# Optimization experiments

Hardware: AMD Instinct MI355X
Metric: run time of the kernel (lower is better)

## Reference

```python
import jax, jax.numpy as jnp
import numpy as np

N, C, T, V, O, S, R = 32, 64, 256, 25, 192, 3, 8  # batch, in_ch, time, joints, out_ch, subsets, rel_ch


def setup_inputs() -> dict:
    key = jax.random.key(0)
    ks = jax.random.split(key, 20)
    w = lambda i, shape: (jax.random.normal(ks[i], shape, jnp.float32) * 0.05)
    return {
        "x": jax.random.normal(ks[0], (N, C, T, V), jnp.float32),
        "spd_A": jax.random.normal(ks[1], (V, V), jnp.float32) * 0.1,
        "A3": jax.random.normal(ks[2], (S, V, V), jnp.float32) * 0.1,
        "A6": jax.random.normal(ks[3], (6, V, V), jnp.float32) * 0.1,
        "conv1_w": w(4, (S, R, C)), "conv1_b": jnp.zeros((S, R), jnp.float32),
        "conv2_w": w(5, (S, R, C)), "conv2_b": jnp.zeros((S, R), jnp.float32),
        "conv4_w": w(6, (S, O, R)), "conv4_b": jnp.zeros((S, O), jnp.float32),
        "conv3_w": w(7, (S, O, C)), "conv3_b": jnp.zeros((S, O), jnp.float32),
        "alpha": jnp.full((1,), 0.5, jnp.float32),
        "beta": jnp.full((1,), 0.5, jnp.float32),
        "gamma": jnp.full((1,), 0.5, jnp.float32),
        "bn_w": jnp.ones((O,), jnp.float32), "bn_b": jnp.zeros((O,), jnp.float32),
        "down_w": w(8, (O, C)), "down_b": jnp.zeros((O,), jnp.float32),
        "dbn_w": jnp.ones((O,), jnp.float32), "dbn_b": jnp.zeros((O,), jnp.float32),
    }


def _bn(y, w, b):
    # BatchNorm2d in training mode: stats over (N, T, V) per channel, biased var
    mu = y.mean(axis=(0, 2, 3), keepdims=True)
    var = ((y - mu) ** 2).mean(axis=(0, 2, 3), keepdims=True)
    return (y - mu) * jax.lax.rsqrt(var + 1e-5) * w[None, :, None, None] + b[None, :, None, None]


def reference(x, spd_A, A3, A6, conv1_w, conv1_b, conv2_w, conv2_b, conv4_w, conv4_b,
              conv3_w, conv3_b, alpha, beta, gamma, bn_w, bn_b, down_w, down_b, dbn_w, dbn_b):
    out_c = conv4_w.shape[1]
    # A6 expanded: (out//6, 6, V, V) -> (out, V, V); contiguous-view == tile along channel blocks
    A6_ex = jnp.tile(A6, (out_c // 6, 1, 1))  # (O, V, V)
    # 1x1 conv then temporal mean == conv on temporal mean (linear op commutes)
    xm = x.mean(axis=2)  # (N, C, V)
    x1 = jnp.einsum('ncv,src->nsrv', xm, conv1_w) + conv1_b[None, :, :, None]
    x2 = jnp.einsum('ncv,src->nsrv', xm, conv2_w) + conv2_b[None, :, :, None]
    d = jnp.tanh(x1[..., :, None] - x2[..., None, :])  # (N, S, R, V, V)
    A_dyn = jnp.einsum('nsruv,sor->nsouv', d, conv4_w) + conv4_b[None, :, :, None, None]
    A_at = (A_dyn * alpha + A3[None, :, None, :, :]
            + A6_ex[None, None] * beta + spd_A[None, None, None] * gamma)  # (N, S, O, V, V)
    # CTRGC_2: x3 = conv3(x); einsum 'ncuv,nctv->nctu', summed over subsets
    x3 = jnp.einsum('nctv,soc->nsotv', x, conv3_w) + conv3_b[None, :, :, None, None]
    y = jnp.einsum('nsouv,nsotv->notu', A_at, x3)  # (N, O, T, V)
    y = _bn(y, bn_w, bn_b)
    xd = jnp.einsum('nctv,oc->notv', x, down_w) + down_b[None, :, None, None]
    y = jax.nn.relu(y + _bn(xd, dbn_w, dbn_b))
    return y
```

## Files before the change

kernel.cpp:

```cpp
#include <hip/hip_runtime.h>

#define N_ 32
#define C_ 64
#define T_ 256
#define V_ 25
#define O_ 192
#define S_ 3
#define R_ 8
#define VV (V_*V_)
#define TV (T_*V_)
#define RP 26
#define TRP (T_*RP)

typedef unsigned short u16;
typedef unsigned int u32;
typedef __attribute__((ext_vector_type(4))) u16 u16x4;
typedef __attribute__((ext_vector_type(8))) u16 u16x8;
typedef __attribute__((ext_vector_type(4))) u32 u32x4;
typedef __attribute__((ext_vector_type(8))) __bf16 bf16x8;
typedef __attribute__((ext_vector_type(4))) float f32x4;

#define WS_A2F_U 0
#define WS_XQ_U  (18874368)
#define WS_XD_U  (18874368 + 13631488)
#define WS_YB_U  (18874368 + 13631488 + 39321600)
#define WS_XM_F   (55574528)
#define WS_RS_F   (55574528 + 51200)
#define WS_STAT_F (55574528 + 51200 + 153600)
#define WS_COEF_F (55574528 + 51200 + 153600 + 768)

__device__ __forceinline__ u16 f2b(float f) {
    return __builtin_bit_cast(u16, (__bf16)f);
}
__device__ __forceinline__ float b2f(u16 u) {
    return __builtin_bit_cast(float, ((unsigned)u) << 16);
}
__device__ __forceinline__ f32x4 mfma16(bf16x8 a, bf16x8 b, f32x4 c) {
    return __builtin_amdgcn_mfma_f32_16x16x32_bf16(a, b, c, 0, 0, 0);
}

__global__ void k0_xq(const float* __restrict__ x, u16* __restrict__ xq) {
    __shared__ float tile[64][52];
    int bid = blockIdx.x;
    int n = bid >> 7, tb = bid & 127;
    int t0 = tb * 2;
    int tid = threadIdx.x;
    const float2* xp = (const float2*)(x + (size_t)n * C_ * TV + t0 * 25);
    for (int p = tid; p < 1600; p += 256) {
        int c = p / 25, q = p % 25;
        float2 f2 = xp[(size_t)c * 3200 + q];
        tile[c][q * 2] = f2.x;
        tile[c][q * 2 + 1] = f2.y;
    }
    __syncthreads();
    for (int p = tid; p < 832; p += 256) {
        int row = p >> 4, c4g = p & 15;
        int t = row >= RP, v = row - t * RP;
        u16x4 w;
        #pragma unroll
        for (int i = 0; i < 4; ++i) {
            int co = ((c4g & 3) << 4) + ((c4g >> 2) << 2) + i;
            w[i] = (v < 25) ? f2b(tile[co][t * 25 + v]) : (u16)0;
        }
        *(u16x4*)&xq[((size_t)n * TRP + tb * 52 + row) * 64 + c4g * 4] = w;
    }
}

__global__ void k1_xm(const u16* __restrict__ xq, float* __restrict__ xm_out) {
    __shared__ float ps[256];
    int bid = blockIdx.x;
    int n = bid / 25, v = bid % 25;
    int tid = threadIdx.x;
    int cg = tid & 63, tg = tid >> 6;
    const u16* p = xq + (size_t)n * TRP * 64 + ((size_t)(tg * 64 * RP + v)) * 64 + cg;
    float s = 0.f;
    for (int t = 0; t < 64; ++t) {
        s += b2f(*p);
        p += RP * 64;
    }
    ps[tid] = s;
    __syncthreads();
    if (tid < 64) {
        float tot = ps[tid] + ps[64 + tid] + ps[128 + tid] + ps[192 + tid];
        int c4g = tid >> 2, i = tid & 3;
        int co = ((c4g & 3) << 4) + ((c4g >> 2) << 2) + i;
        xm_out[((size_t)n * C_ + co) * V_ + v] = tot * (1.f / T_);
    }
}

__global__ void k2_a2f(const float* __restrict__ spd, const float* __restrict__ A3,
                       const float* __restrict__ A6,
                       const float* __restrict__ w1, const float* __restrict__ b1,
                       const float* __restrict__ w2, const float* __restrict__ b2,
                       const float* __restrict__ w4, const float* __restrict__ b4,
                       const float* __restrict__ b3,
                       const float* __restrict__ alpha, const float* __restrict__ beta,
                       const float* __restrict__ gamma,
                       u16* __restrict__ a2f, const float* __restrict__ xmbuf,
                       float* __restrict__ rs_tot) {
    __shared__ float xm[C_ * V_];
    __shared__ float x1s[R_ * V_], x2s[R_ * V_];
    __shared__ float dm[R_ * VV];
    __shared__ float a3s[VV], sps[VV];
    __shared__ float aatw[4][2 * VV];
    int bid = blockIdx.x;
    int n = bid / 24;
    int rem = bid % 24;
    int s = rem / 8, og = rem % 8;
    int tid = threadIdx.x, wid = tid >> 6, lane = tid & 63;
    const float* xmg = xmbuf + (size_t)n * C_ * V_;
    for (int p = tid; p < C_ * V_; p += 256) xm[p] = xmg[p];
    for (int p = tid; p < VV; p += 256) { a3s[p] = A3[s * VV + p]; sps[p] = spd[p]; }
    __syncthreads();
    if (tid < R_ * V_) {
        int r = tid / V_, v = tid % V_;
        float acc1 = b1[s * R_ + r], acc2 = b2[s * R_ + r];
        for (int c = 0; c < C_; ++c) {
            float xv = xm[c * V_ + v];
            acc1 += xv * w1[(s * R_ + r) * C_ + c];
            acc2 += xv * w2[(s * R_ + r) * C_ + c];
        }
        x1s[tid] = acc1; x2s[tid] = acc2;
    }
    __syncthreads();
    for (int p = tid; p < R_ * VV; p += 256) {
        int r = p / VV, uv = p % VV, u = uv / V_, v = uv % V_;
        dm[p] = tanhf(x1s[r * V_ + u] - x2s[r * V_ + v]);
    }
    __syncthreads();
    float al = alpha[0], be = beta[0], ga = gamma[0];
    float* aat = aatw[wid];
    for (int opi = 0; opi < 3; ++opi) {
        int op = wid * 3 + opi;
        int o0 = og * 24 + op * 2;
        float w4v[2][R_], b4v[2];
        #pragma unroll
        for (int oo = 0; oo < 2; ++oo) {
            b4v[oo] = b4[s * O_ + o0 + oo];
            #pragma unroll
            for (int r = 0; r < R_; ++r)
                w4v[oo][r] = w4[((size_t)(s * O_ + o0 + oo)) * R_ + r];
        }
        const float* a6p0 = A6 + ((o0 % 6) * VV);
        for (int p = lane; p < 2 * VV; p += 64) {
            int oo = p / VV, pp = p - oo * VV;
            float acc = b4v[oo];
            #pragma unroll
            for (int r = 0; r < R_; ++r) acc += dm[r * VV + pp] * w4v[oo][r];
            aat[p] = al * acc + a3s[pp] + ga * sps[pp] + be * a6p0[oo * VV + pp];
        }
        if (lane < 2 * V_) {
            int oo = lane / V_, u = lane - oo * V_;
            float rs = 0.f;
            for (int v = 0; v < V_; ++v) rs += aat[oo * VV + u * V_ + v];
            atomicAdd(&rs_tot[((size_t)(n * O_ + o0 + oo)) * V_ + u],
                      b3[s * O_ + o0 + oo] * rs);
        }
        #pragma unroll
        for (int it = 0; it < 4; ++it) {
            int idx = it * 64 + lane;
            int oo = idx >> 7, l2 = idx & 127, cu = l2 >> 6, l = l2 & 63;
            int u = cu * 16 + (l & 15);
            u16x8 w;
            #pragma unroll
            for (int j = 0; j < 8; ++j) {
                int v = ((j >> 2) << 4) + ((l >> 4) << 2) + (j & 3);
                float val = 0.f;
                if (u < V_ && v < V_) val = aat[oo * VV + u * V_ + v];
                w[j] = f2b(val);
            }
            size_t idxg = ((((size_t)(n * O_ + o0 + oo)) * S_ + s) * 2 + cu) * 64 + l;
            ((u16x8*)a2f)[idxg] = w;
        }
    }
}

#define OSTR_B 2504
#define SSTR_B 832
#define BUF_B  20064

__global__ __launch_bounds__(256, 3)
void k3_main(const u16* __restrict__ xq,
             const float* __restrict__ w3, const float* __restrict__ dw,
             const float* __restrict__ db,
             const u16* __restrict__ a2f, const float* __restrict__ rs_tot,
             u16* __restrict__ yb16, u16* __restrict__ xdws,
             float* __restrict__ stats) {
    __shared__ char x3Lb[2 * BUF_B];
    __shared__ u16 xdst[8 * 416];
    __shared__ u16 ystage[8 * 400];
    int orig = blockIdx.x;
    int bid = (orig & 7) * 96 + (orig >> 3);
    int n = bid / 24;
    int o0 = (bid % 24) * 8;
    int tid = threadIdx.x, wid = tid >> 6, lane = tid & 63;
    int lr = lane & 15, lg = lane >> 4;
    int colt = wid & 1;
    int rt0 = (wid >> 1) * 13;

    for (int p = tid; p < 2 * BUF_B / 16; p += 256) ((u32x4*)x3Lb)[p] = u32x4{0,0,0,0};

    const float* wsrc = (colt == 0)
        ? w3 + ((size_t)((lr >> 3) * O_ + o0 + (lr & 7))) * C_
        : ((lr < 8) ? w3 + ((size_t)(2 * O_ + o0 + lr)) * C_
                    : dw + ((size_t)(o0 + lr - 8)) * C_);
    bf16x8 bw[2];
    #pragma unroll
    for (int ks = 0; ks < 2; ++ks) {
        u16x8 tmp;
        #pragma unroll
        for (int j = 0; j < 8; ++j) {
            int c = ks * 32 + (lg << 2) + (j & 3) + ((j >> 2) << 4);
            tmp[j] = f2b(wsrc[c]);
        }
        bw[ks] = __builtin_bit_cast(bf16x8, tmp);
    }
    float dbv = (colt == 1 && lr >= 8) ? db[o0 + lr - 8] : 0.f;

    int wo = (colt == 0) ? (lr & 7) : lr;
    int wsb = (colt == 0) ? (lr >> 3) : 2;
    int colbyte = wo * OSTR_B + wsb * SSTR_B;

    const bf16x8* a2v = (const bf16x8*)a2f;
    bf16x8 Bh[2][6];
    float rsb0[2], rsb1[2];
    #pragma unroll
    for (int oi = 0; oi < 2; ++oi) {
        int o = o0 + (wid << 1) + oi;
        const bf16x8* bp = a2v + ((size_t)(n * O_ + o)) * 6 * 64 + lane;
        #pragma unroll
        for (int q = 0; q < 6; ++q) Bh[oi][q] = bp[(size_t)q * 64];
        const float* rsp = rs_tot + ((size_t)(n * O_ + o)) * V_;
        rsb0[oi] = rsp[lr];
        rsb1[oi] = (lr < 9) ? rsp[16 + lr] : 0.f;
    }

    float sy1[2] = {0, 0}, sy2[2] = {0, 0};
    float sd1 = 0.f, sd2 = 0.f;
    const u16* xbn = xq + (size_t)n * TRP * 64;
    int rdw = 13 * lr + 2 * lg;
    char* buf = x3Lb;
    int t0 = 0;

    auto tl = [&](int ch, int j, u16x8& A0, u16x8& A1) {
        const u16* p = xbn + ((size_t)(ch * 16) * RP + (size_t)((rt0 + j) * 16 + lr)) * 64
                       + (lg << 4);
        A0 = *(const u16x8*)p;
        A1 = *(const u16x8*)(p + 8);
    };
    auto proc = [&](int rt, u16x8 A0, u16x8 A1) {
        f32x4 acc = {0.f, 0.f, 0.f, 0.f};
        acc = mfma16(__builtin_bit_cast(bf16x8, A0), bw[0], acc);
        acc = mfma16(__builtin_bit_cast(bf16x8, A1), bw[1], acc);
        int rbase = rt * 16 + (lg << 2);
        if (colt == 0 || lr < 8) {
            u16x4 w;
            #pragma unroll
            for (int reg = 0; reg < 4; ++reg) w[reg] = f2b(acc[reg]);
            *(u16x4*)(buf + colbyte + rbase * 2) = w;
        } else {
            u16x4 w;
            #pragma unroll
            for (int reg = 0; reg < 4; ++reg) {
                int rr = rbase + reg;
                int t = rr / RP, v = rr - t * RP;
                float val = acc[reg] + dbv;
                w[reg] = f2b(val);
                if (v < 25) { sd1 += val; sd2 += val * val; }
            }
            *(u16x4*)&xdst[(lr - 8) * 416 + rbase] = w;
        }
    };

    __syncthreads();

    u16x8 p0a, p0b, p1a, p1b, p2a, p2b, p3a, p3b;
    tl(0, 0, p0a, p0b); tl(0, 1, p1a, p1b); tl(0, 2, p2a, p2b); tl(0, 3, p3a, p3b);

    for (int ch = 0; ch < 16; ++ch) {
        t0 = ch * 16;
        buf = x3Lb + (ch & 1) * BUF_B;
        proc(rt0 + 0, p0a, p0b);
        proc(rt0 + 1, p1a, p1b);
        proc(rt0 + 2, p2a, p2b);
        proc(rt0 + 3, p3a, p3b);
        for (int j = 4; j < 13; ++j) {
            u16x8 A0, A1;
            tl(ch, j, A0, A1);
            proc(rt0 + j, A0, A1);
        }
        if (ch < 15) {
            tl(ch + 1, 0, p0a, p0b); tl(ch + 1, 1, p1a, p1b);
            tl(ch + 1, 2, p2a, p2b); tl(ch + 1, 3, p3a, p3b);
        }
        __syncthreads();
        #pragma unroll
        for (int oi = 0; oi < 2; ++oi) {
            int ol = (wid << 1) + oi;
            const u32* L = (const u32*)(buf + ol * OSTR_B);
            f32x4 acc0 = {0, 0, 0, 0}, acc1 = {0, 0, 0, 0};
            #pragma unroll
            for (int s = 0; s < 3; ++s) {
                const u32* Ls = L + s * 208 + rdw;
                u32 d0 = Ls[0], d1 = Ls[1], d8 = Ls[8], d9 = Ls[9];
                bf16x8 A = __builtin_bit_cast(bf16x8, u32x4{d0, d1, d8, d9});
                acc0 = mfma16(A, Bh[oi][s * 2 + 0], acc0);
                acc1 = mfma16(A, Bh[oi][s * 2 + 1], acc1);
            }
            int ylb = ol * 400 + (lg << 2) * 25;
            #pragma unroll
            for (int reg = 0; reg < 4; ++reg) {
                float v0 = acc0[reg] + rsb0[oi];
                ystage[ylb + reg * 25 + lr] = f2b(v0);
                sy1[oi] += v0; sy2[oi] += v0 * v0;
                if (lr < 9) {
                    float v1 = acc1[reg] + rsb1[oi];
                    ystage[ylb + reg * 25 + 16 + lr] = f2b(v1);
                    sy1[oi] += v1; sy2[oi] += v1 * v1;
                }
            }
        }
        {
            size_t ygb = (size_t)(n * O_ + o0) * TV + (size_t)t0 * V_;
            for (int q = lane; q < 100; q += 64) {
                int sel = q >= 50;
                int ol2 = (wid << 1) + sel;
                int j = q - sel * 50;
                u16x8 pk = *(const u16x8*)&ystage[ol2 * 400 + j * 8];
                *(u16x8*)&yb16[ygb + (size_t)ol2 * TV + j * 8] = pk;
            }
        }
        if (colt == 1) {
            int tofs = (wid >> 1) * 8;
            size_t gdb = (size_t)(n * O_ + o0) * TV + (size_t)(t0 + tofs) * V_;
            for (int q = lane; q < 200; q += 64) {
                int o = q / 25, w = q - o * 25;
                int g0 = w * 8;
                int tl2 = g0 / 25, v = g0 - tl2 * 25;
                u16x8 pk;
                #pragma unroll
                for (int k = 0; k < 8; ++k) {
                    pk[k] = xdst[o * 416 + (tofs + tl2) * RP + v];
                    if (++v == 25) { v = 0; ++tl2; }
                }
                *(u16x8*)&xdws[gdb + (size_t)o * TV + g0] = pk;
            }
        }
    }
    #pragma unroll
    for (int oi = 0; oi < 2; ++oi) {
        float v1 = sy1[oi], v2 = sy2[oi];
        #pragma unroll
        for (int m = 1; m < 64; m <<= 1) {
            v1 += __shfl_xor(v1, m);
            v2 += __shfl_xor(v2, m);
        }
        if (lane == 0) {
            atomicAdd(&stats[0 * O_ + o0 + (wid << 1) + oi], v1);
            atomicAdd(&stats[1 * O_ + o0 + (wid << 1) + oi], v2);
        }
    }
    if (colt == 1) {
        float v1 = sd1, v2 = sd2;
        v1 += __shfl_xor(v1, 16); v2 += __shfl_xor(v2, 16);
        v1 += __shfl_xor(v1, 32); v2 += __shfl_xor(v2, 32);
        if (lane >= 8 && lane < 16) {
            atomicAdd(&stats[2 * O_ + o0 + lane - 8], v1);
            atomicAdd(&stats[3 * O_ + o0 + lane - 8], v2);
        }
    }
}

__global__ void k4_coef(const float* __restrict__ bn_w, const float* __restrict__ bn_b,
                        const float* __restrict__ dbn_w, const float* __restrict__ dbn_b,
                        const float* __restrict__ stats, float* __restrict__ coef) {
    int o = threadIdx.x;
    if (o >= O_) return;
    float inv = 1.f / (float)(N_ * T_ * V_);
    float mu_y = stats[o] * inv;
    float var_y = stats[O_ + o] * inv - mu_y * mu_y;
    float ay = bn_w[o] * rsqrtf(var_y + 1e-5f);
    float by = bn_b[o] - mu_y * ay;
    float mu_d = stats[2 * O_ + o] * inv;
    float var_d = stats[3 * O_ + o] * inv - mu_d * mu_d;
    float ad = dbn_w[o] * rsqrtf(var_d + 1e-5f);
    float bd = dbn_b[o] - mu_d * ad;
    coef[o] = ay; coef[O_ + o] = by; coef[2 * O_ + o] = ad; coef[3 * O_ + o] = bd;
}

__global__ void k5_final(float* __restrict__ out, const u16* __restrict__ yb,
                         const u16* __restrict__ xd, const float* __restrict__ cf) {
    size_t total = (size_t)N_ * O_ * TV / 8;
    for (size_t i = blockIdx.x * (size_t)blockDim.x + threadIdx.x; i < total;
         i += (size_t)gridDim.x * blockDim.x) {
        int o = (int)((i / 800) % O_);
        float ay = cf[o], by = cf[O_ + o], ad = cf[2 * O_ + o], bd = cf[3 * O_ + o];
        u16x8 yv = ((const u16x8*)yb)[i];
        u16x8 dv = ((const u16x8*)xd)[i];
        float4 r0, r1;
        r0.x = fmaxf(ay * b2f(yv[0]) + by + ad * b2f(dv[0]) + bd, 0.f);
        r0.y = fmaxf(ay * b2f(yv[1]) + by + ad * b2f(dv[1]) + bd, 0.f);
        r0.z = fmaxf(ay * b2f(yv[2]) + by + ad * b2f(dv[2]) + bd, 0.f);
        r0.w = fmaxf(ay * b2f(yv[3]) + by + ad * b2f(dv[3]) + bd, 0.f);
        r1.x = fmaxf(ay * b2f(yv[4]) + by + ad * b2f(dv[4]) + bd, 0.f);
        r1.y = fmaxf(ay * b2f(yv[5]) + by + ad * b2f(dv[5]) + bd, 0.f);
        r1.z = fmaxf(ay * b2f(yv[6]) + by + ad * b2f(dv[6]) + bd, 0.f);
        r1.w = fmaxf(ay * b2f(yv[7]) + by + ad * b2f(dv[7]) + bd, 0.f);
        ((float4*)out)[2 * i] = r0;
        ((float4*)out)[2 * i + 1] = r1;
    }
}

extern "C" void kernel_launch(void* const* d_in, const int* in_sizes, int n_in,
                              void* d_out, int out_size, void* d_ws, size_t ws_size,
                              hipStream_t stream) {
    const float* x     = (const float*)d_in[0];
    const float* spd   = (const float*)d_in[1];
    const float* A3    = (const float*)d_in[2];
    const float* A6    = (const float*)d_in[3];
    const float* w1    = (const float*)d_in[4];
    const float* b1    = (const float*)d_in[5];
    const float* w2    = (const float*)d_in[6];
    const float* b2    = (const float*)d_in[7];
    const float* w4    = (const float*)d_in[8];
    const float* b4    = (const float*)d_in[9];
    const float* w3    = (const float*)d_in[10];
    const float* b3    = (const float*)d_in[11];
    const float* alpha = (const float*)d_in[12];
    const float* beta  = (const float*)d_in[13];
    const float* gamma = (const float*)d_in[14];
    const float* bn_w  = (const float*)d_in[15];
    const float* bn_b  = (const float*)d_in[16];
    const float* dw    = (const float*)d_in[17];
    const float* db    = (const float*)d_in[18];
    const float* dbn_w = (const float*)d_in[19];
    const float* dbn_b = (const float*)d_in[20];
    float* out = (float*)d_out;
    u16*   wsu = (u16*)d_ws;
    float* wsf = (float*)d_ws;

    u16* a2f  = wsu + WS_A2F_U;
    u16* xq   = wsu + WS_XQ_U;
    u16* xd   = wsu + WS_XD_U;
    u16* yb   = wsu + WS_YB_U;
    float* xm    = wsf + WS_XM_F;
    float* rs    = wsf + WS_RS_F;
    float* stats = wsf + WS_STAT_F;
    float* coef  = wsf + WS_COEF_F;

    hipMemsetAsync(rs, 0, (N_ * O_ * V_ + 4 * O_) * sizeof(float), stream);

    k0_xq<<<N_ * 128, 256, 0, stream>>>(x, xq);
    k1_xm<<<N_ * 25, 256, 0, stream>>>(xq, xm);
    k2_a2f<<<N_ * S_ * 8, 256, 0, stream>>>(spd, A3, A6, w1, b1, w2, b2, w4, b4, b3,
                                            alpha, beta, gamma, a2f, xm, rs);
    k3_main<<<N_ * 24, 256, 0, stream>>>(xq, w3, dw, db, a2f, rs, yb, xd, stats);
    k4_coef<<<1, 256, 0, stream>>>(bn_w, bn_b, dbn_w, dbn_b, stats, coef);
    k5_final<<<4096, 256, 0, stream>>>(out, yb, xd, coef);
}
```

Measured before the change: 311.3 us.

## Software-pipeline conv3 GEMM of next chunk with graph-mix GEMM of current chunk

Restructures the main time-chunk loop so that the x3/xd projection for chunk ch+1 (global loads, MFMA, LDS writes into the alternate double buffer) is issued between the xd writeback and the A-mixing MFMA of chunk ch. The explicit register prefetch of four tiles is replaced by this stage skewing, and the per-chunk barrier moves to the end with a manual lgkmcnt wait, raw s_barrier and a sched_barrier. The intent is to overlap global-load latency and the first GEMM with the second GEMM and the stores. The risks are higher register pressure, because the loads are no longer explicitly prefetched, and depending on double-buffer correctness for xdst, which is still a single buffer and is now rewritten by g1 after being read in the same iteration.

Result: no change. 311.2 us (-0.0%).

```diff
diff --git a/kernel.cpp b/kernel.cpp
--- a/kernel.cpp
+++ b/kernel.cpp
@@ -239,97 +239,48 @@
     float sd1 = 0.f, sd2 = 0.f;
     const u16* xbn = xq + (size_t)n * TRP * 64;
     int rdw = 13 * lr + 2 * lg;
-    char* buf = x3Lb;
-    int t0 = 0;
-
-    auto tl = [&](int ch, int j, u16x8& A0, u16x8& A1) {
-        const u16* p = xbn + ((size_t)(ch * 16) * RP + (size_t)((rt0 + j) * 16 + lr)) * 64
-                       + (lg << 4);
-        A0 = *(const u16x8*)p;
-        A1 = *(const u16x8*)(p + 8);
+
+    auto g1 = [&](int ch) {
+        char* bufw = x3Lb + (ch & 1) * BUF_B;
+        for (int j = 0; j < 13; ++j) {
+            const u16* p = xbn + ((size_t)(ch * 16) * RP
+                                  + (size_t)((rt0 + j) * 16 + lr)) * 64 + (lg << 4);
+            u16x8 A0 = *(const u16x8*)p;
+            u16x8 A1 = *(const u16x8*)(p + 8);
+            f32x4 acc = {0.f, 0.f, 0.f, 0.f};
+            acc = mfma16(__builtin_bit_cast(bf16x8, A0), bw[0], acc);
+            acc = mfma16(__builtin_bit_cast(bf16x8, A1), bw[1], acc);
+            int rbase = (rt0 + j) * 16 + (lg << 2);
+            if (colt == 0 || lr < 8) {
+                u16x4 w;
+                #pragma unroll
+                for (int reg = 0; reg < 4; ++reg) w[reg] = f2b(acc[reg]);
+                *(u16x4*)(bufw + colbyte + rbase * 2) = w;
+            } else {
+                u16x4 w;
+                #pragma unroll
+                for (int reg = 0; reg < 4; ++reg) {
+                    int rr = rbase + reg;
+                    int t = rr / RP, v = rr - t * RP;
+                    float val = acc[reg] + dbv;
+                    w[reg] = f2b(val);
+                    if (v < 25) { sd1 += val; sd2 += val * val; }
+                }
+                *(u16x4*)&xdst[(lr - 8) * 416 + rbase] = w;
+            }
+        }
     };
-    auto proc = [&](int rt, u16x8 A0, u16x8 A1) {
-        f32x4 acc = {0.f, 0.f, 0.f, 0.f};
-        acc = mfma16(__builtin_bit_cast(bf16x8, A0), bw[0], acc);
-        acc = mfma16(__builtin_bit_cast(bf16x8, A1), bw[1], acc);
-        int rbase = rt * 16 + (lg << 2);
-        if (colt == 0 || lr < 8) {
-            u16x4 w;
-            #pragma unroll
-            for (int reg = 0; reg < 4; ++reg) w[reg] = f2b(acc[reg]);
-            *(u16x4*)(buf + colbyte + rbase * 2) = w;
-        } else {
-            u16x4 w;
-            #pragma unroll
-            for (int reg = 0; reg < 4; ++reg) {
-                int rr = rbase + reg;
-                int t = rr / RP, v = rr - t * RP;
-                float val = acc[reg] + dbv;
-                w[reg] = f2b(val);
-                if (v < 25) { sd1 += val; sd2 += val * val; }
-            }
-            *(u16x4*)&xdst[(lr - 8) * 416 + rbase] = w;
-        }
-    };
-
-    __syncthreads();
-
-    u16x8 p0a, p0b, p1a, p1b, p2a, p2b, p3a, p3b;
-    tl(0, 0, p0a, p0b); tl(0, 1, p1a, p1b); tl(0, 2, p2a, p2b); tl(0, 3, p3a, p3b);
+
+    __syncthreads();
+
+    g1(0);
+    asm volatile("s_waitcnt lgkmcnt(0)" ::: "memory");
+    __builtin_amdgcn_s_barrier();
+    __builtin_amdgcn_sched_barrier(0);
 
     for (int ch = 0; ch < 16; ++ch) {
-        t0 = ch * 16;
-        buf = x3Lb + (ch & 1) * BUF_B;
-        proc(rt0 + 0, p0a, p0b);
-        proc(rt0 + 1, p1a, p1b);
-        proc(rt0 + 2, p2a, p2b);
-        proc(rt0 + 3, p3a, p3b);
-        for (int j = 4; j < 13; ++j) {
-            u16x8 A0, A1;
-            tl(ch, j, A0, A1);
-            proc(rt0 + j, A0, A1);
-        }
-        if (ch < 15) {
-            tl(ch + 1, 0, p0a, p0b); tl(ch + 1, 1, p1a, p1b);
-            tl(ch + 1, 2, p2a, p2b); tl(ch + 1, 3, p3a, p3b);
-        }
-        __syncthreads();
-        #pragma unroll
-        for (int oi = 0; oi < 2; ++oi) {
-            int ol = (wid << 1) + oi;
-            const u32* L = (const u32*)(buf + ol * OSTR_B);
-            f32x4 acc0 = {0, 0, 0, 0}, acc1 = {0, 0, 0, 0};
-            #pragma unroll
-            for (int s = 0; s < 3; ++s) {
-                const u32* Ls = L + s * 208 + rdw;
-                u32 d0 = Ls[0], d1 = Ls[1], d8 = Ls[8], d9 = Ls[9];
-                bf16x8 A = __builtin_bit_cast(bf16x8, u32x4{d0, d1, d8, d9});
-                acc0 = mfma16(A, Bh[oi][s * 2 + 0], acc0);
-                acc1 = mfma16(A, Bh[oi][s * 2 + 1], acc1);
-            }
-            int ylb = ol * 400 + (lg << 2) * 25;
-            #pragma unroll
-            for (int reg = 0; reg < 4; ++reg) {
-                float v0 = acc0[reg] + rsb0[oi];
-                ystage[ylb + reg * 25 + lr] = f2b(v0);
-                sy1[oi] += v0; sy2[oi] += v0 * v0;
-                if (lr < 9) {
-                    float v1 = acc1[reg] + rsb1[oi];
-                    ystage[ylb + reg * 25 + 16 + lr] = f2b(v1);
-                    sy1[oi] += v1; sy2[oi] += v1 * v1;
-                }
-            }
-        }
-        {
-            size_t ygb = (size_t)(n * O_ + o0) * TV + (size_t)t0 * V_;
-            for (int q = lane; q < 100; q += 64) {
-                int sel = q >= 50;
-                int ol2 = (wid << 1) + sel;
-                int j = q - sel * 50;
-                u16x8 pk = *(const u16x8*)&ystage[ol2 * 400 + j * 8];
-                *(u16x8*)&yb16[ygb + (size_t)ol2 * TV + j * 8] = pk;
-            }
-        }
+        int t0 = ch * 16;
+        char* bufr = x3Lb + (ch & 1) * BUF_B;
         if (colt == 1) {
             int tofs = (wid >> 1) * 8;
             size_t gdb = (size_t)(n * O_ + o0) * TV + (size_t)(t0 + tofs) * V_;
@@ -346,6 +297,46 @@
                 *(u16x8*)&xdws[gdb + (size_t)o * TV + g0] = pk;
             }
         }
+        if (ch < 15) g1(ch + 1);
+        #pragma unroll
+        for (int oi = 0; oi < 2; ++oi) {
+            int ol = (wid << 1) + oi;
+            const u32* L = (const u32*)(bufr + ol * OSTR_B);
+            f32x4 acc0 = {0, 0, 0, 0}, acc1 = {0, 0, 0, 0};
+            #pragma unroll
+            for (int s = 0; s < 3; ++s) {
+                const u32* Ls = L + s * 208 + rdw;
+                u32 d0 = Ls[0], d1 = Ls[1], d8 = Ls[8], d9 = Ls[9];
+                bf16x8 A = __builtin_bit_cast(bf16x8, u32x4{d0, d1, d8, d9});
+                acc0 = mfma16(A, Bh[oi][s * 2 + 0], acc0);
+                acc1 = mfma16(A, Bh[oi][s * 2 + 1], acc1);
+            }
+            int ylb = ol * 400 + (lg << 2) * 25;
+            #pragma unroll
+            for (int reg = 0; reg < 4; ++reg) {
+                float v0 = acc0[reg] + rsb0[oi];
+                ystage[ylb + reg * 25 + lr] = f2b(v0);
+                sy1[oi] += v0; sy2[oi] += v0 * v0;
+                if (lr < 9) {
+                    float v1 = acc1[reg] + rsb1[oi];
+                    ystage[ylb + reg * 25 + 16 + lr] = f2b(v1);
+                    sy1[oi] += v1; sy2[oi] += v1 * v1;
+                }
+            }
+        }
+        {
+            size_t ygb = (size_t)(n * O_ + o0) * TV + (size_t)t0 * V_;
+            for (int q = lane; q < 100; q += 64) {
+                int sel = q >= 50;
+                int ol2 = (wid << 1) + sel;
+                int j = q - sel * 50;
+                u16x8 pk = *(const u16x8*)&ystage[ol2 * 400 + j * 8];
+                *(u16x8*)&yb16[ygb + (size_t)ol2 * TV + j * 8] = pk;
+            }
+        }
+        asm volatile("s_waitcnt lgkmcnt(0)" ::: "memory");
+        __builtin_amdgcn_s_barrier();
+        __builtin_amdgcn_sched_barrier(0);
     }
     #pragma unroll
     for (int oi = 0; oi < 2; ++oi) {
```
